# Optimization experiments

Hardware: AMD Instinct MI355X
Metric: run time of the kernel (lower is better)

## Reference

```python
import jax, jax.numpy as jnp
import numpy as np

D_MODEL = 1024
NHEAD = 16
HEAD_DIM = D_MODEL // NHEAD  # 64
Q_STRIDE = 2
KV_STRIDE = 1
ROPE_BASE = 10000.0


def _rope_tables(positions):
    # positions: [L] int -> cos/sin [L, HEAD_DIM]
    half = HEAD_DIM // 2
    inv_freq = 1.0 / (ROPE_BASE ** (jnp.arange(half, dtype=jnp.float32) / half))
    freqs = positions.astype(jnp.float32)[:, None] * inv_freq[None, :]  # [L, half]
    emb = jnp.concatenate([freqs, freqs], axis=-1)  # [L, HEAD_DIM]
    return jnp.cos(emb), jnp.sin(emb)


def _rotate_half(x):
    half = x.shape[-1] // 2
    return jnp.concatenate([-x[..., half:], x[..., :half]], axis=-1)


def _apply_rope(x, cos, sin):
    # x: [B, H, L, D]; cos/sin: [L, D] broadcast over B, H
    return x * cos + _rotate_half(x) * sin


def setup_inputs() -> dict:
    key = jax.random.key(0)
    ks = jax.random.split(key, 10)
    B, S, K = 4, 1024, 2048
    s = 0.02
    return {
        "query": jax.random.normal(ks[0], (B, S, D_MODEL), jnp.float32),
        "kv": jax.random.normal(ks[1], (B, K, D_MODEL), jnp.float32),
        "q_w": jax.random.normal(ks[2], (D_MODEL, D_MODEL), jnp.float32) * s,
        "q_b": jax.random.normal(ks[3], (D_MODEL,), jnp.float32) * s,
        "k_w": jax.random.normal(ks[4], (D_MODEL, D_MODEL), jnp.float32) * s,
        "k_b": jax.random.normal(ks[5], (D_MODEL,), jnp.float32) * s,
        "v_w": jax.random.normal(ks[6], (D_MODEL, D_MODEL), jnp.float32) * s,
        "v_b": jax.random.normal(ks[7], (D_MODEL,), jnp.float32) * s,
        "out_w": jax.random.normal(ks[8], (D_MODEL, D_MODEL), jnp.float32) * s,
        "out_b": jax.random.normal(ks[9], (D_MODEL,), jnp.float32) * s,
    }


def reference(query, kv, q_w, q_b, k_w, k_b, v_w, v_b, out_w, out_b):
    B, S, _ = query.shape
    K = kv.shape[1]
    # Projections (torch Linear: x @ W^T + b), reshape to [B, H, L, D]
    q = (query @ q_w.T + q_b).reshape(B, S, NHEAD, HEAD_DIM).transpose(0, 2, 1, 3)
    k = (kv @ k_w.T + k_b).reshape(B, K, NHEAD, HEAD_DIM).transpose(0, 2, 1, 3)
    v = (kv @ v_w.T + v_b).reshape(B, K, NHEAD, HEAD_DIM).transpose(0, 2, 1, 3)
    # RoPE at strided original frame positions
    q_cos, q_sin = _rope_tables(jnp.arange(S) * Q_STRIDE)
    k_cos, k_sin = _rope_tables(jnp.arange(K) * KV_STRIDE)
    q = _apply_rope(q, q_cos, q_sin)
    k = _apply_rope(k, k_cos, k_sin)
    scale = 1.0 / np.sqrt(HEAD_DIM).astype(np.float32)
    attn = jnp.einsum('bhsd,bhkd->bhsk', q, k) * scale  # [B, H, S, K]
    attn = jax.nn.softmax(attn, axis=-1)
    out = jnp.einsum('bhsk,bhkd->bhsd', attn, v)
    out = out.transpose(0, 2, 1, 3).reshape(B, S, D_MODEL)
    return out @ out_w.T + out_b
```

## Files before the change

kernel.cpp:

```cpp
#include <hip/hip_runtime.h>
#include <hip/hip_bf16.h>

#define D_MODEL 1024
#define NHEAD   16
#define HD      64
#define SQ      1024
#define SK      2048

typedef __attribute__((ext_vector_type(8))) short bh8;
typedef __attribute__((ext_vector_type(4))) float fx4;

#define QSCALE 0.1803368801111204f

__device__ __forceinline__ unsigned short f2bf(float f) {
  union { float f; unsigned u; } v; v.f = f;
  return (unsigned short)((v.u + 0x7FFFu + ((v.u >> 16) & 1u)) >> 16);
}

__device__ __forceinline__ float bf2f(unsigned short u) {
  union { unsigned u; float f; } v; v.u = ((unsigned)u) << 16; return v.f;
}

#define GLOAD_LDS16(gp, lp)                                                  \
  __builtin_amdgcn_global_load_lds(                                         \
      (const __attribute__((address_space(1))) unsigned int*)(gp),          \
      (__attribute__((address_space(3))) unsigned int*)(lp), 16, 0, 0)

__global__ __launch_bounds__(256) void cvt_kernel(
    const float* __restrict__ q, const float* __restrict__ kv,
    const float* __restrict__ qw, const float* __restrict__ kw,
    const float* __restrict__ vw, const float* __restrict__ ow,
    unsigned short* __restrict__ qx, unsigned short* __restrict__ kvx,
    unsigned short* __restrict__ qwx, unsigned short* __restrict__ kwx,
    unsigned short* __restrict__ vwx, unsigned short* __restrict__ owx)
{
  const int idx = blockIdx.x * 256 + threadIdx.x;
  const float* src; unsigned short* dst; size_t off;
  if (idx < 524288)        { src = q;  dst = qx;  off = idx; }
  else if (idx < 1572864)  { src = kv; dst = kvx; off = idx - 524288; }
  else {
    const int w = idx - 1572864; const int sel = w >> 17; off = w & 131071;
    src = sel == 0 ? qw : sel == 1 ? kw : sel == 2 ? vw : ow;
    dst = sel == 0 ? qwx : sel == 1 ? kwx : sel == 2 ? vwx : owx;
  }
  const float4 a = ((const float4*)src)[off * 2];
  const float4 b = ((const float4*)src)[off * 2 + 1];
  bh8 r;
  r[0] = (short)f2bf(a.x); r[1] = (short)f2bf(a.y);
  r[2] = (short)f2bf(a.z); r[3] = (short)f2bf(a.w);
  r[4] = (short)f2bf(b.x); r[5] = (short)f2bf(b.y);
  r[6] = (short)f2bf(b.z); r[7] = (short)f2bf(b.w);
  *(bh8*)(dst + off * 8) = r;
}

__global__ __launch_bounds__(256) void qkv_kernel(
    const unsigned short* __restrict__ qx, const unsigned short* __restrict__ kvx,
    const unsigned short* __restrict__ qw, const unsigned short* __restrict__ kw,
    const unsigned short* __restrict__ vw,
    const float* __restrict__ qb, const float* __restrict__ kb,
    const float* __restrict__ vb,
    unsigned short* __restrict__ outq, unsigned short* __restrict__ outk,
    unsigned short* __restrict__ outv)
{
  __shared__ unsigned short Alds[2048];
  __shared__ unsigned short Blds[4096];

  const int t = threadIdx.x;
  const int lane = t & 63, w = t >> 6;
  const int lr = lane & 15, g = lane >> 4, kl = g * 8;
  const int bid = blockIdx.x;
  const bool isQ = bid >= 2048;
  int bx, by;
  if (isQ) { const int tq = bid - 2048; bx = tq & 7; by = tq >> 3; }
  else     { bx = bid & 15; by = bid >> 4; }
  const int row0 = by * 64;
  const int colB = bx * 128;
  const int wrow = (w >> 1) * 32;
  const int wcol = (w & 1) * 64;

  const unsigned short* X = isQ ? qx : kvx;
  const unsigned short* Wsrc; const float* bias; int colW; bool isK = false;
  if (isQ)              { Wsrc = qw; bias = qb; colW = colB; }
  else if (colB < 1024) { Wsrc = kw; bias = kb; colW = colB; isK = true; }
  else                  { Wsrc = vw; bias = vb; colW = colB - 1024; }

  const int srow = t >> 2, schunk = (t & 3) * 8;

#define STAGE_P(k0_) do {                                                             \
    GLOAD_LDS16(X + (size_t)(row0 + srow) * 1024 + (k0_) + schunk, &Alds[t * 8]);     \
    GLOAD_LDS16(Wsrc + (size_t)(colW + srow) * 1024 + (k0_) + schunk, &Blds[t * 8]);  \
    GLOAD_LDS16(Wsrc + (size_t)(colW + 64 + srow) * 1024 + (k0_) + schunk,            \
                &Blds[2048 + t * 8]);                                                 \
  } while (0)

  fx4 acc[2][4] = {};
  for (int k0 = 0; k0 < 1024; k0 += 32) {
    __syncthreads();
    STAGE_P(k0);
    __syncthreads();

    bh8 af[2], bf[4];
#pragma unroll
    for (int mi = 0; mi < 2; ++mi)
      af[mi] = *(const bh8*)&Alds[(wrow + mi * 16 + lr) * 32 + kl];
#pragma unroll
    for (int ni = 0; ni < 4; ++ni)
      bf[ni] = *(const bh8*)&Blds[(wcol + ni * 16 + lr) * 32 + kl];
    __builtin_amdgcn_s_setprio(1);
#pragma unroll
    for (int mi = 0; mi < 2; ++mi)
#pragma unroll
      for (int ni = 0; ni < 4; ++ni)
        acc[mi][ni] = __builtin_amdgcn_mfma_f32_16x16x32_bf16(af[mi], bf[ni], acc[mi][ni], 0, 0, 0);
    __builtin_amdgcn_s_setprio(0);
  }

  float bv[4];
#pragma unroll
  for (int ni = 0; ni < 4; ++ni) bv[ni] = bias[colW + wcol + ni * 16 + lr];
#pragma unroll
  for (int mi = 0; mi < 2; ++mi)
#pragma unroll
    for (int ni = 0; ni < 4; ++ni)
#pragma unroll
      for (int j = 0; j < 4; ++j) acc[mi][ni][j] += bv[ni];

  const int LMASK = isQ ? 1023 : 2047;
  if (isQ || isK) {
    const float c0 = 0.41524101186092029f;
    const float invf0 = exp2f(-(float)lr * c0);
    const float invf1 = exp2f(-(float)(16 + lr) * c0);
#pragma unroll
    for (int mi = 0; mi < 2; ++mi)
#pragma unroll
      for (int j = 0; j < 4; ++j) {
        const int rg = row0 + wrow + mi * 16 + 4 * g + j;
        const int s = rg & LMASK;
        const float pos = (float)(isQ ? 2 * s : s);
#pragma unroll
        for (int ni = 0; ni < 2; ++ni) {
          float sn, cs;
          __sincosf(pos * (ni == 0 ? invf0 : invf1), &sn, &cs);
          const float x1 = acc[mi][ni][j], x2 = acc[mi][ni + 2][j];
          acc[mi][ni][j]     = x1 * cs - x2 * sn;
          acc[mi][ni + 2][j] = x2 * cs + x1 * sn;
        }
      }
  }

  const int h = (colW + wcol) >> 6;
#pragma unroll
  for (int mi = 0; mi < 2; ++mi)
#pragma unroll
    for (int j = 0; j < 4; ++j) {
      const int rg = row0 + wrow + mi * 16 + 4 * g + j;
      const int bb = isQ ? (rg >> 10) : (rg >> 11);
      const int s = rg & LMASK;
#pragma unroll
      for (int ni = 0; ni < 4; ++ni) {
        const int d = ni * 16 + lr;
        if (isQ) {
          outq[(((size_t)(bb * 16 + h)) * SQ + s) * 64 + d] = f2bf(acc[mi][ni][j] * QSCALE);
        } else {
          const size_t base = ((size_t)(bb * 16 + h)) * (SK * 64);
          if (isK)
            outk[base + (s >> 4) * 1024 + (d >> 5) * 512 + ((d >> 3) & 3) * 128 + (s & 15) * 8 + (d & 7)]
                = f2bf(acc[mi][ni][j]);
          else
            outv[base + (s >> 5) * 2048 + (d >> 4) * 512 + ((s >> 3) & 3) * 128 + (d & 15) * 8 + (s & 7)]
                = f2bf(acc[mi][ni][j]);
        }
      }
    }
}

__global__ __launch_bounds__(256) void oproj_kernel(
    const unsigned short* __restrict__ A, const unsigned short* __restrict__ W,
    const float* __restrict__ bias, float* __restrict__ out)
{
  __shared__ unsigned short Alds[2048];
  __shared__ unsigned short Blds[4096];

  const int t = threadIdx.x;
  const int lane = t & 63, w = t >> 6;
  const int lr = lane & 15, g = lane >> 4, kl = g * 8;
  const int bid = blockIdx.x;
  const int bx = bid & 7, by = bid >> 3;
  const int row0 = by * 64;
  const int colB = bx * 128;
  const int wrow = (w >> 1) * 32;
  const int wcol = (w & 1) * 64;
  const int srow = t >> 2, schunk = (t & 3) * 8;

#define STAGE_O(k0_) do {                                                             \
    GLOAD_LDS16(A + (size_t)(row0 + srow) * 1024 + (k0_) + schunk, &Alds[t * 8]);     \
    GLOAD_LDS16(W + (size_t)(colB + srow) * 1024 + (k0_) + schunk, &Blds[t * 8]);     \
    GLOAD_LDS16(W + (size_t)(colB + 64 + srow) * 1024 + (k0_) + schunk,               \
                &Blds[2048 + t * 8]);                                                 \
  } while (0)

  fx4 acc[2][4] = {};
  for (int k0 = 0; k0 < 1024; k0 += 32) {
    __syncthreads();
    STAGE_O(k0);
    __syncthreads();

    bh8 af[2], bf[4];
#pragma unroll
    for (int mi = 0; mi < 2; ++mi)
      af[mi] = *(const bh8*)&Alds[(wrow + mi * 16 + lr) * 32 + kl];
#pragma unroll
    for (int ni = 0; ni < 4; ++ni)
      bf[ni] = *(const bh8*)&Blds[(wcol + ni * 16 + lr) * 32 + kl];
    __builtin_amdgcn_s_setprio(1);
#pragma unroll
    for (int mi = 0; mi < 2; ++mi)
#pragma unroll
      for (int ni = 0; ni < 4; ++ni)
        acc[mi][ni] = __builtin_amdgcn_mfma_f32_16x16x32_bf16(af[mi], bf[ni], acc[mi][ni], 0, 0, 0);
    __builtin_amdgcn_s_setprio(0);
  }

  float bv[4];
#pragma unroll
  for (int ni = 0; ni < 4; ++ni) bv[ni] = bias[colB + wcol + ni * 16 + lr];
#pragma unroll
  for (int mi = 0; mi < 2; ++mi)
#pragma unroll
    for (int j = 0; j < 4; ++j) {
      const int rg = row0 + wrow + mi * 16 + 4 * g + j;
#pragma unroll
      for (int ni = 0; ni < 4; ++ni)
        out[(size_t)rg * 1024 + colB + wcol + ni * 16 + lr] = acc[mi][ni][j] + bv[ni];
    }
}

__global__ __launch_bounds__(256, 4) void attn_kernel(
    const unsigned short* __restrict__ Qr, const unsigned short* __restrict__ Kt,
    const unsigned short* __restrict__ Vt, unsigned short* __restrict__ O)
{
  __shared__ __align__(16) unsigned short smem[4 * 2304];
  __shared__ float llds[4][32];

  const int lane = threadIdx.x & 63;
  const int w = threadIdx.x >> 6;
  const int lr = lane & 15, g = lane >> 4, kl = g * 8;
  const int bid = blockIdx.x;
  const int swz = (bid & 7) * 256 + (bid >> 3);
  const int bh = swz >> 5;
  const int q0 = (swz & 31) * 32;
  const int b = bh >> 4, h = bh & 15;

  unsigned short* p_lds = smem + w * 2304;

  const unsigned short* Qp = Qr + (size_t)bh * SQ * HD;
  const unsigned short* Kp = Kt + (size_t)bh * SK * HD;
  const unsigned short* Vp = Vt + (size_t)bh * SK * HD;

  bh8 qf[2][2];
#pragma unroll
  for (int mi = 0; mi < 2; ++mi)
#pragma unroll
    for (int kk = 0; kk < 2; ++kk)
      qf[mi][kk] = *(const bh8*)(Qp + (size_t)(q0 + mi * 16 + lr) * 64 + kk * 32 + kl);

  bh8 ones;
#pragma unroll
  for (int i = 0; i < 8; ++i) ones[i] = (short)0x3F80;

  fx4 oacc[2][4] = {};
  fx4 lacc[2] = {};

  for (int t = 0; t < 8; ++t) {
    fx4 sacc[2][4] = {};
#pragma unroll
    for (int kk = 0; kk < 2; ++kk) {
      bh8 kf[4];
#pragma unroll
      for (int ni = 0; ni < 4; ++ni)
        kf[ni] = *(const bh8*)(Kp + (size_t)(w * 32 + t * 4 + ni) * 1024 + kk * 512 + g * 128 + lr * 8);
      __builtin_amdgcn_s_setprio(1);
#pragma unroll
      for (int mi = 0; mi < 2; ++mi)
#pragma unroll
        for (int ni = 0; ni < 4; ++ni)
          sacc[mi][ni] = __builtin_amdgcn_mfma_f32_16x16x32_bf16(qf[mi][kk], kf[ni], sacc[mi][ni], 0, 0, 0);
      __builtin_amdgcn_s_setprio(0);
    }

    asm volatile("s_waitcnt lgkmcnt(0)" ::: "memory");
    __builtin_amdgcn_sched_barrier(0);

#pragma unroll
    for (int mi = 0; mi < 2; ++mi)
#pragma unroll
      for (int ni = 0; ni < 4; ++ni) {
        float p0, p1, p2, p3;
        asm("v_exp_f32 %0, %1" : "=v"(p0) : "v"(sacc[mi][ni][0]));
        asm("v_exp_f32 %0, %1" : "=v"(p1) : "v"(sacc[mi][ni][1]));
        asm("v_exp_f32 %0, %1" : "=v"(p2) : "v"(sacc[mi][ni][2]));
        asm("v_exp_f32 %0, %1" : "=v"(p3) : "v"(sacc[mi][ni][3]));
        unsigned lo, hi;
        asm("v_cvt_pk_bf16_f32 %0, %1, %2" : "=v"(lo) : "v"(p0), "v"(p1));
        asm("v_cvt_pk_bf16_f32 %0, %1, %2" : "=v"(hi) : "v"(p2), "v"(p3));
        unsigned short* base = &p_lds[(mi * 16 + 4 * g) * 68 + ni * 16 + lr];
        base[0]   = (unsigned short)lo;
        base[68]  = (unsigned short)(lo >> 16);
        base[136] = (unsigned short)hi;
        base[204] = (unsigned short)(hi >> 16);
      }

    asm volatile("s_waitcnt lgkmcnt(0)" ::: "memory");
    __builtin_amdgcn_sched_barrier(0);

#pragma unroll
    for (int kk = 0; kk < 2; ++kk) {
      bh8 pa[2], vb[4];
#pragma unroll
      for (int mi = 0; mi < 2; ++mi) {
        const unsigned short* pp = &p_lds[(mi * 16 + lr) * 68 + kk * 32 + kl];
        const short4 a = *(const short4*)pp;
        const short4 c = *(const short4*)(pp + 4);
        pa[mi][0] = a.x; pa[mi][1] = a.y; pa[mi][2] = a.z; pa[mi][3] = a.w;
        pa[mi][4] = c.x; pa[mi][5] = c.y; pa[mi][6] = c.z; pa[mi][7] = c.w;
      }
#pragma unroll
      for (int ni = 0; ni < 4; ++ni)
        vb[ni] = *(const bh8*)(Vp + (size_t)(w * 16 + t * 2 + kk) * 2048 + ni * 512 + g * 128 + lr * 8);
      __builtin_amdgcn_s_setprio(1);
#pragma unroll
      for (int mi = 0; mi < 2; ++mi) {
#pragma unroll
        for (int ni = 0; ni < 4; ++ni)
          oacc[mi][ni] = __builtin_amdgcn_mfma_f32_16x16x32_bf16(pa[mi], vb[ni], oacc[mi][ni], 0, 0, 0);
        lacc[mi] = __builtin_amdgcn_mfma_f32_16x16x32_bf16(pa[mi], ones, lacc[mi], 0, 0, 0);
      }
      __builtin_amdgcn_s_setprio(0);
    }
  }

  if (lr == 0) {
#pragma unroll
    for (int mi = 0; mi < 2; ++mi)
#pragma unroll
      for (int j = 0; j < 4; ++j)
        llds[w][mi * 16 + 4 * g + j] = lacc[mi][j];
  }

  asm volatile("s_waitcnt lgkmcnt(0)" ::: "memory");
  __builtin_amdgcn_sched_barrier(0);
  unsigned short* opart = smem + w * 2304;
#pragma unroll
  for (int mi = 0; mi < 2; ++mi)
#pragma unroll
    for (int j = 0; j < 4; ++j) {
      const int row = mi * 16 + 4 * g + j;
#pragma unroll
      for (int ni = 0; ni < 4; ++ni)
        opart[row * 72 + ni * 16 + lr] = f2bf(oacc[mi][ni][j]);
    }
  __syncthreads();

  const int row = threadIdx.x >> 3;
  const int d0 = (threadIdx.x & 7) * 8;
  float a8[8] = {};
#pragma unroll
  for (int ww = 0; ww < 4; ++ww) {
    const bh8 v = *(const bh8*)(smem + ww * 2304 + row * 72 + d0);
#pragma unroll
    for (int i = 0; i < 8; ++i) a8[i] += bf2f((unsigned short)v[i]);
  }
  const float inv = 1.0f / (llds[0][row] + llds[1][row] + llds[2][row] + llds[3][row]);
  bh8 r;
#pragma unroll
  for (int i = 0; i < 8; ++i) r[i] = (short)f2bf(a8[i] * inv);
  *(bh8*)&O[((size_t)(b * SQ + q0 + row)) * D_MODEL + h * 64 + d0] = r;
}

extern "C" void kernel_launch(void* const* d_in, const int* in_sizes, int n_in,
                              void* d_out, int out_size, void* d_ws, size_t ws_size,
                              hipStream_t stream) {
  (void)in_sizes; (void)n_in; (void)out_size; (void)ws_size;
  const float* query = (const float*)d_in[0];
  const float* kv    = (const float*)d_in[1];
  const float* q_w   = (const float*)d_in[2];
  const float* q_b   = (const float*)d_in[3];
  const float* k_w   = (const float*)d_in[4];
  const float* k_b   = (const float*)d_in[5];
  const float* v_w   = (const float*)d_in[6];
  const float* v_b   = (const float*)d_in[7];
  const float* out_w = (const float*)d_in[8];
  const float* out_b = (const float*)d_in[9];
  float* out = (float*)d_out;

  unsigned short* ws = (unsigned short*)d_ws;
  unsigned short* qx     = ws;
  unsigned short* kvx    = ws + ((size_t)4  << 20);
  unsigned short* qwx    = ws + ((size_t)12 << 20);
  unsigned short* kwx    = ws + ((size_t)13 << 20);
  unsigned short* vwx    = ws + ((size_t)14 << 20);
  unsigned short* owx    = ws + ((size_t)15 << 20);
  unsigned short* q_rope = ws + ((size_t)16 << 20);
  unsigned short* k_t    = ws + ((size_t)20 << 20);
  unsigned short* v_t    = ws + ((size_t)28 << 20);
  unsigned short* attn_o = qx;

  hipLaunchKernelGGL(cvt_kernel, dim3(8192), dim3(256), 0, stream,
                     query, kv, q_w, k_w, v_w, out_w, qx, kvx, qwx, kwx, vwx, owx);
  hipLaunchKernelGGL(qkv_kernel, dim3(2560), dim3(256), 0, stream,
                     qx, kvx, qwx, kwx, vwx, q_b, k_b, v_b, q_rope, k_t, v_t);
  hipLaunchKernelGGL(attn_kernel, dim3(2048), dim3(256), 0, stream,
                     q_rope, k_t, v_t, attn_o);
  hipLaunchKernelGGL(oproj_kernel, dim3(512), dim3(256), 0, stream,
                     attn_o, owx, out_b, out);
}
```

Baseline: 167.5 us.

## Enlarge GEMM tiles to 128x128xK64 with XOR-swizzled LDS in projections

The QKV projection kernel now uses 128x128 output tiles with a K step of 64, so each wave computes a 64x64 sub-tile and loads more data per barrier. The launch grid is halved to match. The output projection also moves to a K step of 64. Both kernels stage tiles into LDS with an XOR swizzle, applied through the global address of each row chunk and mirrored on the fragment reads, to avoid bank conflicts. This cuts the number of barriers and global loads per FLOP, but raises register pressure (acc grows to 4x4) and LDS use per block, which may reduce occupancy.

```diff
diff --git a/kernel.cpp b/kernel.cpp
--- a/kernel.cpp
+++ b/kernel.cpp
@@ -62,20 +62,20 @@
     unsigned short* __restrict__ outq, unsigned short* __restrict__ outk,
     unsigned short* __restrict__ outv)
 {
-  __shared__ unsigned short Alds[2048];
-  __shared__ unsigned short Blds[4096];
+  __shared__ unsigned short Alds[8192];
+  __shared__ unsigned short Blds[8192];
 
   const int t = threadIdx.x;
   const int lane = t & 63, w = t >> 6;
-  const int lr = lane & 15, g = lane >> 4, kl = g * 8;
+  const int lr = lane & 15, g = lane >> 4;
   const int bid = blockIdx.x;
-  const bool isQ = bid >= 2048;
+  const bool isQ = bid >= 1024;
   int bx, by;
-  if (isQ) { const int tq = bid - 2048; bx = tq & 7; by = tq >> 3; }
+  if (isQ) { const int tq = bid - 1024; bx = tq & 7; by = tq >> 3; }
   else     { bx = bid & 15; by = bid >> 4; }
-  const int row0 = by * 64;
+  const int row0 = by * 128;
   const int colB = bx * 128;
-  const int wrow = (w >> 1) * 32;
+  const int wrow = (w >> 1) * 64;
   const int wcol = (w & 1) * 64;
 
   const unsigned short* X = isQ ? qx : kvx;
@@ -84,42 +84,50 @@
   else if (colB < 1024) { Wsrc = kw; bias = kb; colW = colB; isK = true; }
   else                  { Wsrc = vw; bias = vb; colW = colB - 1024; }
 
-  const int srow = t >> 2, schunk = (t & 3) * 8;
-
-#define STAGE_P(k0_) do {                                                             \
-    GLOAD_LDS16(X + (size_t)(row0 + srow) * 1024 + (k0_) + schunk, &Alds[t * 8]);     \
-    GLOAD_LDS16(Wsrc + (size_t)(colW + srow) * 1024 + (k0_) + schunk, &Blds[t * 8]);  \
-    GLOAD_LDS16(Wsrc + (size_t)(colW + 64 + srow) * 1024 + (k0_) + schunk,            \
-                &Blds[2048 + t * 8]);                                                 \
-  } while (0)
-
-  fx4 acc[2][4] = {};
-  for (int k0 = 0; k0 < 1024; k0 += 32) {
+  const int rbase = t >> 3;
+  const int sw8 = (((t & 7) ^ (rbase & 7))) * 8;
+
+  const int sl0 = ((g) ^ (lr & 7)) * 8;
+  const int sl1 = ((4 + g) ^ (lr & 7)) * 8;
+
+  fx4 acc[4][4] = {};
+  for (int k0 = 0; k0 < 1024; k0 += 64) {
     __syncthreads();
-    STAGE_P(k0);
+#pragma unroll
+    for (int l = 0; l < 4; ++l)
+      GLOAD_LDS16(X + (size_t)(row0 + rbase + l * 32) * 1024 + k0 + sw8,
+                  &Alds[l * 2048 + t * 8]);
+#pragma unroll
+    for (int l = 0; l < 4; ++l)
+      GLOAD_LDS16(Wsrc + (size_t)(colW + rbase + l * 32) * 1024 + k0 + sw8,
+                  &Blds[l * 2048 + t * 8]);
     __syncthreads();
 
-    bh8 af[2], bf[4];
-#pragma unroll
-    for (int mi = 0; mi < 2; ++mi)
-      af[mi] = *(const bh8*)&Alds[(wrow + mi * 16 + lr) * 32 + kl];
-#pragma unroll
-    for (int ni = 0; ni < 4; ++ni)
-      bf[ni] = *(const bh8*)&Blds[(wcol + ni * 16 + lr) * 32 + kl];
-    __builtin_amdgcn_s_setprio(1);
-#pragma unroll
-    for (int mi = 0; mi < 2; ++mi)
-#pragma unroll
-      for (int ni = 0; ni < 4; ++ni)
-        acc[mi][ni] = __builtin_amdgcn_mfma_f32_16x16x32_bf16(af[mi], bf[ni], acc[mi][ni], 0, 0, 0);
-    __builtin_amdgcn_s_setprio(0);
+#pragma unroll
+    for (int kk = 0; kk < 2; ++kk) {
+      const int sl = kk ? sl1 : sl0;
+      bh8 af[4], bf[4];
+#pragma unroll
+      for (int mi = 0; mi < 4; ++mi)
+        af[mi] = *(const bh8*)&Alds[(wrow + mi * 16 + lr) * 64 + sl];
+#pragma unroll
+      for (int ni = 0; ni < 4; ++ni)
+        bf[ni] = *(const bh8*)&Blds[(wcol + ni * 16 + lr) * 64 + sl];
+      __builtin_amdgcn_s_setprio(1);
+#pragma unroll
+      for (int mi = 0; mi < 4; ++mi)
+#pragma unroll
+        for (int ni = 0; ni < 4; ++ni)
+          acc[mi][ni] = __builtin_amdgcn_mfma_f32_16x16x32_bf16(af[mi], bf[ni], acc[mi][ni], 0, 0, 0);
+      __builtin_amdgcn_s_setprio(0);
+    }
   }
 
   float bv[4];
 #pragma unroll
   for (int ni = 0; ni < 4; ++ni) bv[ni] = bias[colW + wcol + ni * 16 + lr];
 #pragma unroll
-  for (int mi = 0; mi < 2; ++mi)
+  for (int mi = 0; mi < 4; ++mi)
 #pragma unroll
     for (int ni = 0; ni < 4; ++ni)
 #pragma unroll
@@ -131,7 +139,7 @@
     const float invf0 = exp2f(-(float)lr * c0);
     const float invf1 = exp2f(-(float)(16 + lr) * c0);
 #pragma unroll
-    for (int mi = 0; mi < 2; ++mi)
+    for (int mi = 0; mi < 4; ++mi)
 #pragma unroll
       for (int j = 0; j < 4; ++j) {
         const int rg = row0 + wrow + mi * 16 + 4 * g + j;
@@ -150,7 +158,7 @@
 
   const int h = (colW + wcol) >> 6;
 #pragma unroll
-  for (int mi = 0; mi < 2; ++mi)
+  for (int mi = 0; mi < 4; ++mi)
 #pragma unroll
     for (int j = 0; j < 4; ++j) {
       const int rg = row0 + wrow + mi * 16 + 4 * g + j;
@@ -178,47 +186,55 @@
     const unsigned short* __restrict__ A, const unsigned short* __restrict__ W,
     const float* __restrict__ bias, float* __restrict__ out)
 {
-  __shared__ unsigned short Alds[2048];
-  __shared__ unsigned short Blds[4096];
+  __shared__ unsigned short Alds[4096];
+  __shared__ unsigned short Blds[8192];
 
   const int t = threadIdx.x;
   const int lane = t & 63, w = t >> 6;
-  const int lr = lane & 15, g = lane >> 4, kl = g * 8;
+  const int lr = lane & 15, g = lane >> 4;
   const int bid = blockIdx.x;
   const int bx = bid & 7, by = bid >> 3;
   const int row0 = by * 64;
   const int colB = bx * 128;
   const int wrow = (w >> 1) * 32;
   const int wcol = (w & 1) * 64;
-  const int srow = t >> 2, schunk = (t & 3) * 8;
-
-#define STAGE_O(k0_) do {                                                             \
-    GLOAD_LDS16(A + (size_t)(row0 + srow) * 1024 + (k0_) + schunk, &Alds[t * 8]);     \
-    GLOAD_LDS16(W + (size_t)(colB + srow) * 1024 + (k0_) + schunk, &Blds[t * 8]);     \
-    GLOAD_LDS16(W + (size_t)(colB + 64 + srow) * 1024 + (k0_) + schunk,               \
-                &Blds[2048 + t * 8]);                                                 \
-  } while (0)
+
+  const int rbase = t >> 3;
+  const int sw8 = (((t & 7) ^ (rbase & 7))) * 8;
+  const int sl0 = ((g) ^ (lr & 7)) * 8;
+  const int sl1 = ((4 + g) ^ (lr & 7)) * 8;
 
   fx4 acc[2][4] = {};
-  for (int k0 = 0; k0 < 1024; k0 += 32) {
+  for (int k0 = 0; k0 < 1024; k0 += 64) {
     __syncthreads();
-    STAGE_O(k0);
+#pragma unroll
+    for (int l = 0; l < 2; ++l)
+      GLOAD_LDS16(A + (size_t)(row0 + rbase + l * 32) * 1024 + k0 + sw8,
+                  &Alds[l * 2048 + t * 8]);
+#pragma unroll
+    for (int l = 0; l < 4; ++l)
+      GLOAD_LDS16(W + (size_t)(colB + rbase + l * 32) * 1024 + k0 + sw8,
+                  &Blds[l * 2048 + t * 8]);
     __syncthreads();
 
-    bh8 af[2], bf[4];
-#pragma unroll
-    for (int mi = 0; mi < 2; ++mi)
-      af[mi] = *(const bh8*)&Alds[(wrow + mi * 16 + lr) * 32 + kl];
-#pragma unroll
-    for (int ni = 0; ni < 4; ++ni)
-      bf[ni] = *(const bh8*)&Blds[(wcol + ni * 16 + lr) * 32 + kl];
-    __builtin_amdgcn_s_setprio(1);
-#pragma unroll
-    for (int mi = 0; mi < 2; ++mi)
-#pragma unroll
-      for (int ni = 0; ni < 4; ++ni)
-        acc[mi][ni] = __builtin_amdgcn_mfma_f32_16x16x32_bf16(af[mi], bf[ni], acc[mi][ni], 0, 0, 0);
-    __builtin_amdgcn_s_setprio(0);
+#pragma unroll
+    for (int kk = 0; kk < 2; ++kk) {
+      const int sl = kk ? sl1 : sl0;
+      bh8 af[2], bf[4];
+#pragma unroll
+      for (int mi = 0; mi < 2; ++mi)
+        af[mi] = *(const bh8*)&Alds[(wrow + mi * 16 + lr) * 64 + sl];
+#pragma unroll
+      for (int ni = 0; ni < 4; ++ni)
+        bf[ni] = *(const bh8*)&Blds[(wcol + ni * 16 + lr) * 64 + sl];
+      __builtin_amdgcn_s_setprio(1);
+#pragma unroll
+      for (int mi = 0; mi < 2; ++mi)
+#pragma unroll
+        for (int ni = 0; ni < 4; ++ni)
+          acc[mi][ni] = __builtin_amdgcn_mfma_f32_16x16x32_bf16(af[mi], bf[ni], acc[mi][ni], 0, 0, 0);
+      __builtin_amdgcn_s_setprio(0);
+    }
   }
 
   float bv[4];
@@ -407,7 +423,7 @@
 
   hipLaunchKernelGGL(cvt_kernel, dim3(8192), dim3(256), 0, stream,
                      query, kv, q_w, k_w, v_w, out_w, qx, kvx, qwx, kwx, vwx, owx);
-  hipLaunchKernelGGL(qkv_kernel, dim3(2560), dim3(256), 0, stream,
+  hipLaunchKernelGGL(qkv_kernel, dim3(1280), dim3(256), 0, stream,
                      qx, kvx, qwx, kwx, vwx, q_b, k_b, v_b, q_rope, k_t, v_t);
   hipLaunchKernelGGL(attn_kernel, dim3(2048), dim3(256), 0, stream,
                      q_rope, k_t, v_t, attn_o);
```

Result: faster. 158.7 us (-5.3%).

## Triple-buffer LDS with async prefetch, swizzle LDS chunks, remap block order in GEMMs

Applied to the files above, without the earlier changes.

The QKV and output-projection GEMMs now use a three-stage LDS ring buffer. Loads are issued two k-tiles ahead, with explicit vmcnt waits and a single barrier per iteration, replacing the two syncthreads per tile. The 16-byte chunk positions within each LDS row are XOR-swizzled on both the store and load side to reduce bank conflicts. Block IDs are remapped so that neighbouring blocks share weight column tiles for better L2 reuse. LDS use triples, which may lower occupancy.

```diff
diff --git a/kernel.cpp b/kernel.cpp
--- a/kernel.cpp
+++ b/kernel.cpp
@@ -62,17 +62,23 @@
     unsigned short* __restrict__ outq, unsigned short* __restrict__ outk,
     unsigned short* __restrict__ outv)
 {
-  __shared__ unsigned short Alds[2048];
-  __shared__ unsigned short Blds[4096];
+  __shared__ unsigned short Alds[3 * 2048];
+  __shared__ unsigned short Blds[3 * 4096];
 
   const int t = threadIdx.x;
   const int lane = t & 63, w = t >> 6;
-  const int lr = lane & 15, g = lane >> 4, kl = g * 8;
+  const int lr = lane & 15, g = lane >> 4;
   const int bid = blockIdx.x;
   const bool isQ = bid >= 2048;
   int bx, by;
-  if (isQ) { const int tq = bid - 2048; bx = tq & 7; by = tq >> 3; }
-  else     { bx = bid & 15; by = bid >> 4; }
+  if (isQ) {
+    const int tq = bid - 2048;
+    const int nq = (tq & 7) * 64 + (tq >> 3);
+    bx = nq & 7; by = nq >> 3;
+  } else {
+    const int nk = (bid & 7) * 256 + (bid >> 3);
+    bx = nk & 15; by = nk >> 4;
+  }
   const int row0 = by * 64;
   const int colB = bx * 128;
   const int wrow = (w >> 1) * 32;
@@ -84,28 +90,38 @@
   else if (colB < 1024) { Wsrc = kw; bias = kb; colW = colB; isK = true; }
   else                  { Wsrc = vw; bias = vb; colW = colB - 1024; }
 
-  const int srow = t >> 2, schunk = (t & 3) * 8;
-
-#define STAGE_P(k0_) do {                                                             \
-    GLOAD_LDS16(X + (size_t)(row0 + srow) * 1024 + (k0_) + schunk, &Alds[t * 8]);     \
-    GLOAD_LDS16(Wsrc + (size_t)(colW + srow) * 1024 + (k0_) + schunk, &Blds[t * 8]);  \
-    GLOAD_LDS16(Wsrc + (size_t)(colW + 64 + srow) * 1024 + (k0_) + schunk,            \
-                &Blds[2048 + t * 8]);                                                 \
+  const int srow = t >> 2;
+  const int gch8 = (((t & 3) ^ ((t >> 3) & 3))) * 8;
+  const int sl8 = ((g ^ ((lr >> 1) & 3))) * 8;
+
+#define STAGE_P(k0_, bi_) do {                                                        \
+    GLOAD_LDS16(X + (size_t)(row0 + srow) * 1024 + (k0_) + gch8,                      \
+                &Alds[(bi_) * 2048 + t * 8]);                                         \
+    GLOAD_LDS16(Wsrc + (size_t)(colW + srow) * 1024 + (k0_) + gch8,                   \
+                &Blds[(bi_) * 4096 + t * 8]);                                         \
+    GLOAD_LDS16(Wsrc + (size_t)(colW + 64 + srow) * 1024 + (k0_) + gch8,              \
+                &Blds[(bi_) * 4096 + 2048 + t * 8]);                                  \
   } while (0)
 
   fx4 acc[2][4] = {};
-  for (int k0 = 0; k0 < 1024; k0 += 32) {
-    __syncthreads();
-    STAGE_P(k0);
-    __syncthreads();
+  STAGE_P(0, 0);
+  STAGE_P(32, 1);
+  for (int kt = 0; kt < 32; ++kt) {
+    const int cb = kt % 3;
+    if (kt < 31) asm volatile("s_waitcnt vmcnt(3)" ::: "memory");
+    else         asm volatile("s_waitcnt vmcnt(0)" ::: "memory");
+    __builtin_amdgcn_sched_barrier(0);
+    __builtin_amdgcn_s_barrier();
+    __builtin_amdgcn_sched_barrier(0);
+    if (kt < 30) STAGE_P((kt + 2) * 32, (kt + 2) % 3);
 
     bh8 af[2], bf[4];
 #pragma unroll
     for (int mi = 0; mi < 2; ++mi)
-      af[mi] = *(const bh8*)&Alds[(wrow + mi * 16 + lr) * 32 + kl];
+      af[mi] = *(const bh8*)&Alds[cb * 2048 + (wrow + mi * 16 + lr) * 32 + sl8];
 #pragma unroll
     for (int ni = 0; ni < 4; ++ni)
-      bf[ni] = *(const bh8*)&Blds[(wcol + ni * 16 + lr) * 32 + kl];
+      bf[ni] = *(const bh8*)&Blds[cb * 4096 + (wcol + ni * 16 + lr) * 32 + sl8];
     __builtin_amdgcn_s_setprio(1);
 #pragma unroll
     for (int mi = 0; mi < 2; ++mi)
@@ -178,40 +194,52 @@
     const unsigned short* __restrict__ A, const unsigned short* __restrict__ W,
     const float* __restrict__ bias, float* __restrict__ out)
 {
-  __shared__ unsigned short Alds[2048];
-  __shared__ unsigned short Blds[4096];
+  __shared__ unsigned short Alds[3 * 2048];
+  __shared__ unsigned short Blds[3 * 4096];
 
   const int t = threadIdx.x;
   const int lane = t & 63, w = t >> 6;
-  const int lr = lane & 15, g = lane >> 4, kl = g * 8;
+  const int lr = lane & 15, g = lane >> 4;
   const int bid = blockIdx.x;
-  const int bx = bid & 7, by = bid >> 3;
+  const int nb = (bid & 7) * 64 + (bid >> 3);
+  const int bx = nb & 7, by = nb >> 3;
   const int row0 = by * 64;
   const int colB = bx * 128;
   const int wrow = (w >> 1) * 32;
   const int wcol = (w & 1) * 64;
-  const int srow = t >> 2, schunk = (t & 3) * 8;
-
-#define STAGE_O(k0_) do {                                                             \
-    GLOAD_LDS16(A + (size_t)(row0 + srow) * 1024 + (k0_) + schunk, &Alds[t * 8]);     \
-    GLOAD_LDS16(W + (size_t)(colB + srow) * 1024 + (k0_) + schunk, &Blds[t * 8]);     \
-    GLOAD_LDS16(W + (size_t)(colB + 64 + srow) * 1024 + (k0_) + schunk,               \
-                &Blds[2048 + t * 8]);                                                 \
+
+  const int srow = t >> 2;
+  const int gch8 = (((t & 3) ^ ((t >> 3) & 3))) * 8;
+  const int sl8 = ((g ^ ((lr >> 1) & 3))) * 8;
+
+#define STAGE_O(k0_, bi_) do {                                                        \
+    GLOAD_LDS16(A + (size_t)(row0 + srow) * 1024 + (k0_) + gch8,                      \
+                &Alds[(bi_) * 2048 + t * 8]);                                         \
+    GLOAD_LDS16(W + (size_t)(colB + srow) * 1024 + (k0_) + gch8,                      \
+                &Blds[(bi_) * 4096 + t * 8]);                                         \
+    GLOAD_LDS16(W + (size_t)(colB + 64 + srow) * 1024 + (k0_) + gch8,                 \
+                &Blds[(bi_) * 4096 + 2048 + t * 8]);                                  \
   } while (0)
 
   fx4 acc[2][4] = {};
-  for (int k0 = 0; k0 < 1024; k0 += 32) {
-    __syncthreads();
-    STAGE_O(k0);
-    __syncthreads();
+  STAGE_O(0, 0);
+  STAGE_O(32, 1);
+  for (int kt = 0; kt < 32; ++kt) {
+    const int cb = kt % 3;
+    if (kt < 31) asm volatile("s_waitcnt vmcnt(3)" ::: "memory");
+    else         asm volatile("s_waitcnt vmcnt(0)" ::: "memory");
+    __builtin_amdgcn_sched_barrier(0);
+    __builtin_amdgcn_s_barrier();
+    __builtin_amdgcn_sched_barrier(0);
+    if (kt < 30) STAGE_O((kt + 2) * 32, (kt + 2) % 3);
 
     bh8 af[2], bf[4];
 #pragma unroll
     for (int mi = 0; mi < 2; ++mi)
-      af[mi] = *(const bh8*)&Alds[(wrow + mi * 16 + lr) * 32 + kl];
+      af[mi] = *(const bh8*)&Alds[cb * 2048 + (wrow + mi * 16 + lr) * 32 + sl8];
 #pragma unroll
     for (int ni = 0; ni < 4; ++ni)
-      bf[ni] = *(const bh8*)&Blds[(wcol + ni * 16 + lr) * 32 + kl];
+      bf[ni] = *(const bh8*)&Blds[cb * 4096 + (wcol + ni * 16 + lr) * 32 + sl8];
     __builtin_amdgcn_s_setprio(1);
 #pragma unroll
     for (int mi = 0; mi < 2; ++mi)
```

New measurement: 160.5 us. 4.2% less time.
